# Performance work log

Measured on AMD Instinct MI355X. Metric: run time of the kernel, lower is better.

The kernel has to match this reference:

```python
import jax, jax.numpy as jnp
import numpy as np

BS, NA, NE_, NL = 128, 3, 3, 3
NALL = NA - 1                 # n_allies
ENT = NA + NE_ + NL           # 9 entities
EM1 = ENT - 1                 # 8
HID = 64                      # hidden_dim
HEAD = 4
HIN = 9                       # hyper input dim
HYP = 64                      # hyper hidden dim
NRBF, RUB = 3, 10.0
EPS = 1e-7


def _lin_init(k, fan_in, fan_out):
    k1, k2 = jax.random.split(k)
    lim = 1.0 / np.sqrt(fan_in)
    w = jax.random.uniform(k1, (fan_in, fan_out), minval=-lim, maxval=lim, dtype=jnp.float32)
    b = jax.random.uniform(k2, (fan_out,), minval=-lim, maxval=lim, dtype=jnp.float32)
    return w, b


def setup_inputs():
    key = jax.random.key(0)
    ks = jax.random.split(key, 12)
    d = {}
    obs_dim = 4 + 2 * (NL + NALL + NE_) + 2 * (NALL + NE_)  # 30
    d["inputs"] = jax.random.normal(ks[0], (BS * NA, obs_dim), dtype=jnp.float32)
    d["hidden_state"] = jnp.zeros((1, HID), dtype=jnp.float32)
    d["actions"] = jax.random.normal(ks[1], (BS * NA, 2), dtype=jnp.float32)
    out_dim = (HIN + 1) * HID * HEAD  # 2560
    d["hA1_w"], d["hA1_b"] = _lin_init(ks[2], HIN, HYP)
    d["hA2_w"], d["hA2_b"] = _lin_init(ks[3], HYP, out_dim)
    d["hE1_w"], d["hE1_b"] = _lin_init(ks[4], HIN, HYP)
    d["hE2_w"], d["hE2_b"] = _lin_init(ks[5], HYP, out_dim)
    d["hL1_w"], d["hL1_b"] = _lin_init(ks[6], HIN, HYP)
    d["hL2_w"], d["hL2_b"] = _lin_init(ks[7], HYP, out_dim)
    d["merger_w"] = jnp.ones((1, HEAD, HID), dtype=jnp.float32)
    d["fc1_w"], d["fc1_b"] = _lin_init(ks[8], HID + 3, HID)
    d["fc2_w"], d["fc2_b"] = _lin_init(ks[9], HID, 1)
    return d


def _pair_out(feat, w1, b1, w2, b2):
    # hypernetwork: Linear(9,64) -> LeakyReLU -> Linear(64, (9+1)*64*4)
    h = jax.nn.leaky_relu(feat @ w1 + b1, negative_slope=0.01)
    out = h @ w2 + b2                               # (bs,NA,EM1,EM1,2560)
    nw = HIN * HID * HEAD
    w = out[..., :nw].reshape(feat.shape[:-1] + (HIN, HID * HEAD))
    b = out[..., nw:]
    y = jnp.einsum('...k,...kd->...d', feat, w) + b  # tiny 1x9 @ 9x256 per pair
    return y.reshape(feat.shape[:-1] + (HEAD, HID))


def _forward(inputs, actions, hA1_w, hA1_b, hA2_w, hA2_b, hE1_w, hE1_b, hE2_w, hE2_b,
             hL1_w, hL1_b, hL2_w, hL2_b, merger_w, fc1_w, fc1_b, fc2_w, fc2_b):
    bs = inputs.shape[0] // NA
    ob = inputs
    own = ob[:, :4].reshape(bs, NA, 4)
    i = 4
    lm_pos = ob[:, i:i + NL * 2].reshape(bs, NA, NL, 2); i += NL * 2
    ally_pos = ob[:, i:i + NALL * 2].reshape(bs, NA, NALL, 2); i += NALL * 2
    enemy_pos = ob[:, i:i + NE_ * 2].reshape(bs, NA, NE_, 2); i += NE_ * 2
    entity_pos = jnp.concatenate([ally_pos, enemy_pos, lm_pos], axis=-2)  # (bs,NA,EM1,2)
    ally_vel = ob[:, i:i + NALL * 2].reshape(bs, NA, NALL, 2); i += NALL * 2
    enemy_vel = ob[:, i:i + NE_ * 2].reshape(bs, NA, NE_, 2)
    lm_vel = jnp.zeros_like(lm_pos) - own[:, :, None, :2]
    entity_vel = jnp.concatenate([ally_vel, enemy_vel, lm_vel], axis=-2)  # (bs,NA,EM1,2)
    # rel_vel[b,a,j,i] = vel[i] - vel[j]
    rel_vel = entity_vel[:, :, None, :, :] - entity_vel[:, :, :, None, :]
    vel_norm = jnp.sqrt((entity_vel ** 2).sum(-1))
    sin_a = entity_vel[..., 1] / (vel_norm + EPS)
    cos_a = entity_vel[..., 0] / (vel_norm + EPS)
    act = actions.reshape(bs, NA, 2)
    act_norm = jnp.sqrt((act ** 2).sum(-1))        # (bs,NA)
    sin_b = act[..., 1] / (act_norm + EPS)
    cos_b = act[..., 0] / (act_norm + EPS)
    dist = jnp.sqrt((entity_pos ** 2).sum(-1))     # (bs,NA,EM1)
    sin_t = entity_pos[..., 1] / (dist + EPS)
    cos_t = entity_pos[..., 0] / (dist + EPS)
    # pair angles: A,C vary over last axis (i), B over second-to-last (j)
    sA, cA = sin_t[:, :, None, :], cos_t[:, :, None, :]
    sB, cB = sin_t[:, :, :, None], cos_t[:, :, :, None]
    sC, cC = sin_a[:, :, None, :], cos_a[:, :, None, :]
    angle_info = jnp.stack([sA * cB - cA * sB, cA * cB + sA * sB,
                            sC * cB - cC * sB, cC * cB + sC * sB], axis=-1)
    angle_info = jnp.broadcast_to(angle_info, (bs, NA, EM1, EM1, 4))
    sD, cD = sin_b[:, :, None], cos_b[:, :, None]
    act_angle = jnp.stack([sD * cos_t - cD * sin_t, cD * cos_t + sD * sin_t], axis=-1)  # (bs,NA,EM1,2)
    # gaussian RBF (schnet-style smearing, num_rbf=3, rbound_upper=10)
    offset = jnp.linspace(0.0, RUB, NRBF)
    coeff = -0.5 / (offset[1] - offset[0]) ** 2
    rbf = jnp.exp(coeff * (dist[..., None] - offset) ** 2)  # (bs,NA,EM1,NRBF)
    feat_dist = jnp.broadcast_to(rbf[:, :, None, :, :], (bs, NA, EM1, EM1, NRBF))
    feat = jnp.concatenate([feat_dist, angle_info, rel_vel], axis=-1)  # (bs,NA,EM1,EM1,9)
    ally_out = _pair_out(feat, hA1_w, hA1_b, hA2_w, hA2_b)
    enemy_out = _pair_out(feat, hE1_w, hE1_b, hE2_w, hE2_b)
    lm_out = _pair_out(feat, hL1_w, hL1_b, hL2_w, hL2_b)
    # type-based selection over the source-entity axis (dim 3), then sum-aggregate
    m = jnp.concatenate([ally_out[:, :, :, :NALL],
                         enemy_out[:, :, :, NALL:NALL + NE_],
                         lm_out[:, :, :, NALL + NE_:]], axis=3)
    m_sum = m.sum(axis=3)                               # (bs,NA,EM1,HEAD,HID)
    mw = jax.nn.softmax(merger_w, axis=1)               # (1,HEAD,HID)
    m_jki = (mw * m_sum).sum(axis=-2)                   # (bs,NA,EM1,HID)
    an = jnp.broadcast_to(act_norm[:, :, None], (bs, NA, EM1))[..., None]
    final = jnp.concatenate([m_jki, an, act_angle], axis=-1)  # (bs,NA,EM1,HID+3)
    x = jax.nn.relu(final)
    x = jax.nn.relu(x @ fc1_w + fc1_b)
    q = (x @ fc2_w + fc2_b).mean(axis=-2).reshape(-1, 1)  # (bs*NA,1)
    return q, x


def reference(inputs, hidden_state, actions, hA1_w, hA1_b, hA2_w, hA2_b,
              hE1_w, hE1_b, hE2_w, hE2_b, hL1_w, hL1_b, hL2_w, hL2_b,
              merger_w, fc1_w, fc1_b, fc2_w, fc2_b):
    q, x = _forward(inputs, actions, hA1_w, hA1_b, hA2_w, hA2_b,
                    hE1_w, hE1_b, hE2_w, hE2_b, hL1_w, hL1_b, hL2_w, hL2_b,
                    merger_w, fc1_w, fc1_b, fc2_w, fc2_b)
    return q, x
```

## Files before the change

### kernel.cpp

```cpp
#include <hip/hip_runtime.h>
#include <math.h>

#define EPS 1e-7f
#define NETS 3
#define HROWP 384
#define HG    (HROWP/4)
#define GPW   (HG/4)
#define JSTRIDE (NETS*HROWP)
#define W2R_F4_TOT (2*NETS*HG*64)

__global__ __launch_bounds__(256) void prep_w2r(
    const float* __restrict__ W2A, const float* __restrict__ b2A,
    const float* __restrict__ W2E, const float* __restrict__ b2E,
    const float* __restrict__ W2L, const float* __restrict__ b2L,
    const float* __restrict__ merger, float* __restrict__ W2r)
{
    int idx = blockIdx.x * 256 + threadIdx.x;
    if (idx >= W2R_F4_TOT) return;
    int half = idx / (NETS*HG*64);
    int rem  = idx - half * (NETS*HG*64);
    int net  = rem / (HG*64);
    rem     -= net * (HG*64);
    int g4   = rem >> 6;
    int hid  = rem & 63;

    float m0 = merger[hid], m1 = merger[64+hid], m2 = merger[128+hid], m3 = merger[192+hid];
    float mx = fmaxf(fmaxf(m0, m1), fmaxf(m2, m3));
    float e0 = expf(m0-mx), e1 = expf(m1-mx), e2 = expf(m2-mx), e3 = expf(m3-mx);
    float inv = 1.0f / (e0+e1+e2+e3);
    float w0 = e0*inv, w1 = e1*inv, w2 = e2*inv, w3 = e3*inv;

    const float* W2 = (net==0) ? W2A : ((net==1) ? W2E : W2L);
    const float* b2 = (net==0) ? b2A : ((net==1) ? b2E : b2L);

    float4 v;
    float* vp = &v.x;
    #pragma unroll
    for (int r = 0; r < 4; ++r) {
        int row = g4*4 + r;
        float val = 0.0f;
        if (row < 325) {
            const float* src;
            int kk;
            if (row < 320) { kk = half*5 + (row >> 6); int h = row & 63; src = W2 + h*2560; }
            else           { kk = half*5 + (row - 320);                  src = b2; }
            int col = (kk < 9) ? kk*256 : 2304;
            val = w0*src[col+hid] + w1*src[col+64+hid] + w2*src[col+128+hid] + w3*src[col+192+hid];
        }
        vp[r] = val;
    }
    ((float4*)W2r)[idx] = v;
}

__global__ __launch_bounds__(256, 3) void half_kernel(
    const float* __restrict__ inputs, const float* __restrict__ actions,
    const float* __restrict__ W1A, const float* __restrict__ b1A,
    const float* __restrict__ W1E, const float* __restrict__ b1E,
    const float* __restrict__ W1L, const float* __restrict__ b1L,
    const float* __restrict__ W2r, float* __restrict__ Zpart)
{
    __shared__ float sOb[32];
    __shared__ float sSt[8], sCt[8], sSa[8], sCa[8], sVx[8], sVy[8];
    __shared__ float sRbf[8][3];
    __shared__ float sF[64][10];
    __shared__ __align__(16) float sU[8 * JSTRIDE];
    __shared__ float sZp[4][8][64];

    const int tid   = threadIdx.x;
    const int agent = blockIdx.x >> 1;
    const int half  = blockIdx.x & 1;

    if (tid < 30) sOb[tid] = inputs[agent*30 + tid];
    if (tid == 30) sOb[30] = actions[agent*2 + 0];
    if (tid == 31) sOb[31] = actions[agent*2 + 1];
    __syncthreads();

    if (tid < 8) {
        int e = tid;
        float px, py, vx, vy;
        if (e < 2)      {           px = sOb[10+2*e]; py = sOb[11+2*e]; vx = sOb[20+2*e]; vy = sOb[21+2*e]; }
        else if (e < 5) { int t=e-2; px = sOb[14+2*t]; py = sOb[15+2*t]; vx = sOb[24+2*t]; vy = sOb[25+2*t]; }
        else            { int t=e-5; px = sOb[4+2*t];  py = sOb[5+2*t];  vx = -sOb[0];     vy = -sOb[1]; }
        float d  = sqrtf(px*px + py*py);
        sSt[e] = py / (d + EPS);
        sCt[e] = px / (d + EPS);
        float vn = sqrtf(vx*vx + vy*vy);
        sSa[e] = vy / (vn + EPS);
        sCa[e] = vx / (vn + EPS);
        sVx[e] = vx; sVy[e] = vy;
        sRbf[e][0] = expf(-0.02f * d * d);
        float d5  = d - 5.0f;  sRbf[e][1] = expf(-0.02f * d5  * d5);
        float d10 = d - 10.0f; sRbf[e][2] = expf(-0.02f * d10 * d10);
    }
    __syncthreads();

    if (tid < 64) {
        int p = tid, j = p >> 3, k = p & 7;
        sF[p][0] = sRbf[k][0];
        sF[p][1] = sRbf[k][1];
        sF[p][2] = sRbf[k][2];
        sF[p][3] = sSt[k]*sCt[j] - sCt[k]*sSt[j];
        sF[p][4] = sCt[k]*sCt[j] + sSt[k]*sSt[j];
        sF[p][5] = sSa[k]*sCt[j] - sCa[k]*sSt[j];
        sF[p][6] = sCa[k]*sCt[j] + sSa[k]*sSt[j];
        sF[p][7] = sVx[k] - sVx[j];
        sF[p][8] = sVy[k] - sVy[j];
        sF[p][9] = 1.0f;
    }
    __syncthreads();

    for (int e = tid; e < 1536; e += 256) {
        int j = e / 192, rem = e - j*192;
        int net = rem >> 6, r = rem & 63;
        float v = 0.0f;
        if (r < 5) {
            int kk = half*5 + r;
            int ks = (net==0) ? 0 : ((net==1) ? 2 : 5);
            int kn = (net==0) ? 2 : 3;
            for (int q = 0; q < kn; ++q) v += sF[j*8 + ks + q][kk];
        }
        sU[(j*NETS + net)*HROWP + 320 + r] = v;
    }
    for (int e = tid; e < 1536; e += 256) {
        int j = e / 192, rem = e - j*192;
        int net = rem >> 6, h = rem & 63;
        int ks = (net==0) ? 0 : ((net==1) ? 2 : 5);
        int kn = (net==0) ? 2 : 3;
        const float* W1 = (net==0) ? W1A : ((net==1) ? W1E : W1L);
        const float* b1 = (net==0) ? b1A : ((net==1) ? b1E : b1L);
        float v[5];
        #pragma unroll
        for (int c = 0; c < 5; ++c) v[c] = 0.0f;
        for (int q = 0; q < kn; ++q) {
            int p = j*8 + ks + q;
            float acc = b1[h];
            #pragma unroll
            for (int kk = 0; kk < 9; ++kk) acc = fmaf(sF[p][kk], W1[kk*64 + h], acc);
            float H = (acc > 0.0f) ? acc : 0.01f*acc;
            #pragma unroll
            for (int c = 0; c < 5; ++c) v[c] = fmaf(H, sF[p][half*5 + c], v[c]);
        }
        float* dst = sU + (j*NETS + net)*HROWP + h;
        #pragma unroll
        for (int c = 0; c < 5; ++c) dst[c*64] = v[c];
    }
    __syncthreads();

    {
        const int lane = tid & 63, w = tid >> 6;
        const int q = lane >> 4, hh = lane & 15;
        const int base = w * GPW;
        float acc[8][4];
        #pragma unroll
        for (int j = 0; j < 8; ++j)
            #pragma unroll
            for (int k = 0; k < 4; ++k) acc[j][k] = 0.0f;

        const float4* Wbase = (const float4*)W2r + (size_t)half * (NETS*HG*64);

        float4 wk0, wk1, wk2, wk3, cu[8];
        {
            int g = base + q;
            const float4* wb = Wbase + g*64 + hh;
            wk0 = wb[0]; wk1 = wb[16]; wk2 = wb[32]; wk3 = wb[48];
            const float* Ub = sU + g*4;
            #pragma unroll
            for (int j = 0; j < 8; ++j) cu[j] = *(const float4*)(Ub + j*JSTRIDE);
        }
        for (int it = 0; it < 18; ++it) {
            float4 nk0, nk1, nk2, nk3, nu[8];
            if (it < 17) {
                int nit = it + 1;
                int nnet = nit / 6, nu_ = nit - nnet*6;
                int ng = base + nu_*4 + q;
                const float4* wb = Wbase + (nnet*HG + ng)*64 + hh;
                nk0 = wb[0]; nk1 = wb[16]; nk2 = wb[32]; nk3 = wb[48];
                const float* Ub = sU + nnet*HROWP + ng*4;
                #pragma unroll
                for (int j = 0; j < 8; ++j) nu[j] = *(const float4*)(Ub + j*JSTRIDE);
            }
            #pragma unroll
            for (int j = 0; j < 8; ++j) {
                float4 uu = cu[j];
                acc[j][0] = fmaf(uu.x,wk0.x, fmaf(uu.y,wk0.y, fmaf(uu.z,wk0.z, fmaf(uu.w,wk0.w, acc[j][0]))));
                acc[j][1] = fmaf(uu.x,wk1.x, fmaf(uu.y,wk1.y, fmaf(uu.z,wk1.z, fmaf(uu.w,wk1.w, acc[j][1]))));
                acc[j][2] = fmaf(uu.x,wk2.x, fmaf(uu.y,wk2.y, fmaf(uu.z,wk2.z, fmaf(uu.w,wk2.w, acc[j][2]))));
                acc[j][3] = fmaf(uu.x,wk3.x, fmaf(uu.y,wk3.y, fmaf(uu.z,wk3.z, fmaf(uu.w,wk3.w, acc[j][3]))));
            }
            wk0 = nk0; wk1 = nk1; wk2 = nk2; wk3 = nk3;
            #pragma unroll
            for (int j = 0; j < 8; ++j) cu[j] = nu[j];
        }
        #pragma unroll
        for (int j = 0; j < 8; ++j) {
            #pragma unroll
            for (int k = 0; k < 4; ++k) {
                float v = acc[j][k];
                v += __shfl_xor(v, 16);
                v += __shfl_xor(v, 32);
                if (q == 0) sZp[w][j][k*16 + hh] = v;
            }
        }
    }
    __syncthreads();
    {
        float* dst = Zpart + (size_t)agent*1024 + half*512;
        for (int o = tid; o < 512; o += 256) {
            int j = o >> 6, c = o & 63;
            dst[o] = sZp[0][j][c] + sZp[1][j][c] + sZp[2][j][c] + sZp[3][j][c];
        }
    }
}

__global__ __launch_bounds__(256) void epilogue_kernel(
    const float* __restrict__ inputs, const float* __restrict__ actions,
    const float* __restrict__ Zpart,
    const float* __restrict__ fc1w, const float* __restrict__ fc1b,
    const float* __restrict__ fc2w, const float* __restrict__ fc2b,
    float* __restrict__ out_q, float* __restrict__ out_x)
{
    __shared__ float sOb[32];
    __shared__ float sSt[8], sCt[8];
    __shared__ float sAct[3];
    __shared__ float sZ[8][64];
    __shared__ float sRed[4];

    const int tid   = threadIdx.x;
    const int agent = blockIdx.x;

    if (tid < 30) sOb[tid] = inputs[agent*30 + tid];
    if (tid == 30) sOb[30] = actions[agent*2 + 0];
    if (tid == 31) sOb[31] = actions[agent*2 + 1];
    __syncthreads();

    if (tid < 8) {
        int e = tid;
        float px, py;
        if (e < 2)      {           px = sOb[10+2*e]; py = sOb[11+2*e]; }
        else if (e < 5) { int t=e-2; px = sOb[14+2*t]; py = sOb[15+2*t]; }
        else            { int t=e-5; px = sOb[4+2*t];  py = sOb[5+2*t]; }
        float d = sqrtf(px*px + py*py);
        sSt[e] = py / (d + EPS);
        sCt[e] = px / (d + EPS);
    }
    if (tid == 8) {
        float ax = sOb[30], ay = sOb[31];
        float an = sqrtf(ax*ax + ay*ay);
        sAct[0] = an;
        sAct[1] = ay / (an + EPS);
        sAct[2] = ax / (an + EPS);
    }
    const float* Zp = Zpart + (size_t)agent*1024;
    for (int o = tid; o < 512; o += 256) {
        float z = Zp[o] + Zp[512 + o];
        ((float*)sZ)[o] = (z > 0.0f) ? z : 0.0f;
    }
    __syncthreads();

    float an  = sAct[0], sb = sAct[1], cb = sAct[2];
    float anr = (an > 0.0f) ? an : 0.0f;
    float myq = 0.0f;
    #pragma unroll
    for (int i = 0; i < 2; ++i) {
        int o = i*256 + tid;
        int j = o >> 6, c = o & 63;
        float acc = fc1b[c];
        #pragma unroll 8
        for (int d = 0; d < 64; ++d)
            acc = fmaf(sZ[j][d], fc1w[d*64 + c], acc);
        float aa0 = sb*sCt[j] - cb*sSt[j];
        float aa1 = cb*sCt[j] + sb*sSt[j];
        aa0 = (aa0 > 0.0f) ? aa0 : 0.0f;
        aa1 = (aa1 > 0.0f) ? aa1 : 0.0f;
        acc = fmaf(anr, fc1w[64*64 + c], acc);
        acc = fmaf(aa0, fc1w[65*64 + c], acc);
        acc = fmaf(aa1, fc1w[66*64 + c], acc);
        float x1 = (acc > 0.0f) ? acc : 0.0f;
        out_x[(agent*8 + j)*64 + c] = x1;
        myq = fmaf(x1, fc2w[c], myq);
    }
    for (int off = 32; off; off >>= 1) myq += __shfl_down(myq, off);
    int lane = tid & 63, w = tid >> 6;
    if (lane == 0) sRed[w] = myq;
    __syncthreads();
    if (tid == 0) out_q[agent] = (sRed[0] + sRed[1] + sRed[2] + sRed[3]) * 0.125f + fc2b[0];
}

extern "C" void kernel_launch(void* const* d_in, const int* in_sizes, int n_in,
                              void* d_out, int out_size, void* d_ws, size_t ws_size,
                              hipStream_t stream) {
    const float* inputs  = (const float*)d_in[0];
    const float* actions = (const float*)d_in[2];
    const float* hA1_w = (const float*)d_in[3];  const float* hA1_b = (const float*)d_in[4];
    const float* hA2_w = (const float*)d_in[5];  const float* hA2_b = (const float*)d_in[6];
    const float* hE1_w = (const float*)d_in[7];  const float* hE1_b = (const float*)d_in[8];
    const float* hE2_w = (const float*)d_in[9];  const float* hE2_b = (const float*)d_in[10];
    const float* hL1_w = (const float*)d_in[11]; const float* hL1_b = (const float*)d_in[12];
    const float* hL2_w = (const float*)d_in[13]; const float* hL2_b = (const float*)d_in[14];
    const float* merger = (const float*)d_in[15];
    const float* fc1w = (const float*)d_in[16];  const float* fc1b = (const float*)d_in[17];
    const float* fc2w = (const float*)d_in[18];  const float* fc2b = (const float*)d_in[19];

    float* W2r   = (float*)d_ws;
    float* Zpart = (float*)((char*)d_ws + 589824);
    float* q     = (float*)d_out;
    float* x     = q + 384;

    prep_w2r<<<(W2R_F4_TOT + 255)/256, 256, 0, stream>>>(
        hA2_w, hA2_b, hE2_w, hE2_b, hL2_w, hL2_b, merger, W2r);
    half_kernel<<<768, 256, 0, stream>>>(
        inputs, actions, hA1_w, hA1_b, hE1_w, hE1_b, hL1_w, hL1_b, W2r, Zpart);
    epilogue_kernel<<<384, 256, 0, stream>>>(
        inputs, actions, Zpart, fc1w, fc1b, fc2w, fc2b, q, x);
}
```

Measured before the change: 122.1 us.

## Fuse epilogue into half kernel via last-block atomic counter

Removes the separate epilogue launch. The second of the two half-blocks per agent, detected with an atomic counter, now sums the partial Z and runs fc1/fc2. It also stages the W1/b1 weights in shared memory and merges the two sU-fill loops into one pass. The main loop now reads the U operands straight from shared memory each iteration instead of prefetching them into registers, which lowers register pressure. The cost is fences and atomics, the counter reset folded into prep_w2r, extra shared memory for sW1, and more LDS traffic in the inner loop.

```diff
diff --git a/kernel.cpp b/kernel.cpp
--- a/kernel.cpp
+++ b/kernel.cpp
@@ -8,14 +8,18 @@
 #define GPW   (HG/4)
 #define JSTRIDE (NETS*HROWP)
 #define W2R_F4_TOT (2*NETS*HG*64)
+#define ZPART_OFF 589824
+#define ZCNT_OFF  2162688
 
 __global__ __launch_bounds__(256) void prep_w2r(
     const float* __restrict__ W2A, const float* __restrict__ b2A,
     const float* __restrict__ W2E, const float* __restrict__ b2E,
     const float* __restrict__ W2L, const float* __restrict__ b2L,
-    const float* __restrict__ merger, float* __restrict__ W2r)
+    const float* __restrict__ merger, float* __restrict__ W2r,
+    int* __restrict__ Zcnt)
 {
     int idx = blockIdx.x * 256 + threadIdx.x;
+    if (idx < 384) Zcnt[idx] = 0;
     if (idx >= W2R_F4_TOT) return;
     int half = idx / (NETS*HG*64);
     int rem  = idx - half * (NETS*HG*64);
@@ -57,14 +61,21 @@
     const float* __restrict__ W1A, const float* __restrict__ b1A,
     const float* __restrict__ W1E, const float* __restrict__ b1E,
     const float* __restrict__ W1L, const float* __restrict__ b1L,
-    const float* __restrict__ W2r, float* __restrict__ Zpart)
+    const float* __restrict__ W2r, float* __restrict__ Zpart,
+    int* __restrict__ Zcnt,
+    const float* __restrict__ fc1w, const float* __restrict__ fc1b,
+    const float* __restrict__ fc2w, const float* __restrict__ fc2b,
+    float* __restrict__ out_q, float* __restrict__ out_x)
 {
     __shared__ float sOb[32];
     __shared__ float sSt[8], sCt[8], sSa[8], sCa[8], sVx[8], sVy[8];
     __shared__ float sRbf[8][3];
+    __shared__ float sAct[3];
     __shared__ float sF[64][10];
+    __shared__ float sW1[NETS*640];
     __shared__ __align__(16) float sU[8 * JSTRIDE];
-    __shared__ float sZp[4][8][64];
+    __shared__ float sRed[4];
+    __shared__ int   sIsLast;
 
     const int tid   = threadIdx.x;
     const int agent = blockIdx.x >> 1;
@@ -73,6 +84,13 @@
     if (tid < 30) sOb[tid] = inputs[agent*30 + tid];
     if (tid == 30) sOb[30] = actions[agent*2 + 0];
     if (tid == 31) sOb[31] = actions[agent*2 + 1];
+    for (int i = tid; i < 480; i += 256) {
+        int net = i / 160, r = i - net*160;
+        const float* W1 = (net==0) ? W1A : ((net==1) ? W1E : W1L);
+        const float* b1 = (net==0) ? b1A : ((net==1) ? b1E : b1L);
+        const float4 v = (r < 144) ? ((const float4*)W1)[r] : ((const float4*)b1)[r-144];
+        ((float4*)(sW1 + net*640))[r] = v;
+    }
     __syncthreads();
 
     if (tid < 8) {
@@ -92,6 +110,13 @@
         float d5  = d - 5.0f;  sRbf[e][1] = expf(-0.02f * d5  * d5);
         float d10 = d - 10.0f; sRbf[e][2] = expf(-0.02f * d10 * d10);
     }
+    if (tid == 8) {
+        float ax = sOb[30], ay = sOb[31];
+        float an = sqrtf(ax*ax + ay*ay);
+        sAct[0] = an;
+        sAct[1] = ay / (an + EPS);
+        sAct[2] = ax / (an + EPS);
+    }
     __syncthreads();
 
     if (tid < 64) {
@@ -109,43 +134,45 @@
     }
     __syncthreads();
 
-    for (int e = tid; e < 1536; e += 256) {
-        int j = e / 192, rem = e - j*192;
-        int net = rem >> 6, r = rem & 63;
-        float v = 0.0f;
-        if (r < 5) {
-            int kk = half*5 + r;
+    for (int e = tid; e < 3072; e += 256) {
+        if (e < 1536) {
+            int j = e / 192, rem = e - j*192;
+            int net = rem >> 6, h = rem & 63;
             int ks = (net==0) ? 0 : ((net==1) ? 2 : 5);
             int kn = (net==0) ? 2 : 3;
-            for (int q = 0; q < kn; ++q) v += sF[j*8 + ks + q][kk];
-        }
-        sU[(j*NETS + net)*HROWP + 320 + r] = v;
-    }
-    for (int e = tid; e < 1536; e += 256) {
-        int j = e / 192, rem = e - j*192;
-        int net = rem >> 6, h = rem & 63;
-        int ks = (net==0) ? 0 : ((net==1) ? 2 : 5);
-        int kn = (net==0) ? 2 : 3;
-        const float* W1 = (net==0) ? W1A : ((net==1) ? W1E : W1L);
-        const float* b1 = (net==0) ? b1A : ((net==1) ? b1E : b1L);
-        float v[5];
-        #pragma unroll
-        for (int c = 0; c < 5; ++c) v[c] = 0.0f;
-        for (int q = 0; q < kn; ++q) {
-            int p = j*8 + ks + q;
-            float acc = b1[h];
-            #pragma unroll
-            for (int kk = 0; kk < 9; ++kk) acc = fmaf(sF[p][kk], W1[kk*64 + h], acc);
-            float H = (acc > 0.0f) ? acc : 0.01f*acc;
-            #pragma unroll
-            for (int c = 0; c < 5; ++c) v[c] = fmaf(H, sF[p][half*5 + c], v[c]);
-        }
-        float* dst = sU + (j*NETS + net)*HROWP + h;
-        #pragma unroll
-        for (int c = 0; c < 5; ++c) dst[c*64] = v[c];
-    }
-    __syncthreads();
-
+            const float* w1 = sW1 + net*640;
+            float v[5];
+            #pragma unroll
+            for (int c = 0; c < 5; ++c) v[c] = 0.0f;
+            for (int q = 0; q < kn; ++q) {
+                int p = j*8 + ks + q;
+                float acc = w1[576 + h];
+                #pragma unroll
+                for (int kk = 0; kk < 9; ++kk) acc = fmaf(sF[p][kk], w1[kk*64 + h], acc);
+                float H = (acc > 0.0f) ? acc : 0.01f*acc;
+                #pragma unroll
+                for (int c = 0; c < 5; ++c) v[c] = fmaf(H, sF[p][half*5 + c], v[c]);
+            }
+            float* dst = sU + (j*NETS + net)*HROWP + h;
+            #pragma unroll
+            for (int c = 0; c < 5; ++c) dst[c*64] = v[c];
+        } else {
+            int t = e - 1536;
+            int j = t / 192, rem = t - j*192;
+            int net = rem >> 6, r = rem & 63;
+            float v = 0.0f;
+            if (r < 5) {
+                int kk = half*5 + r;
+                int ks = (net==0) ? 0 : ((net==1) ? 2 : 5);
+                int kn = (net==0) ? 2 : 3;
+                for (int q = 0; q < kn; ++q) v += sF[j*8 + ks + q][kk];
+            }
+            sU[(j*NETS + net)*HROWP + 320 + r] = v;
+        }
+    }
+    __syncthreads();
+
+    float vr[8][4];
     {
         const int lane = tid & 63, w = tid >> 6;
         const int q = lane >> 4, hh = lane & 15;
@@ -157,133 +184,111 @@
             for (int k = 0; k < 4; ++k) acc[j][k] = 0.0f;
 
         const float4* Wbase = (const float4*)W2r + (size_t)half * (NETS*HG*64);
-
-        float4 wk0, wk1, wk2, wk3, cu[8];
-        {
-            int g = base + q;
+        float4 wk0, wk1, wk2, wk3;
+        {   int g = base + q;
             const float4* wb = Wbase + g*64 + hh;
-            wk0 = wb[0]; wk1 = wb[16]; wk2 = wb[32]; wk3 = wb[48];
-            const float* Ub = sU + g*4;
-            #pragma unroll
-            for (int j = 0; j < 8; ++j) cu[j] = *(const float4*)(Ub + j*JSTRIDE);
-        }
+            wk0 = wb[0]; wk1 = wb[16]; wk2 = wb[32]; wk3 = wb[48]; }
+
         for (int it = 0; it < 18; ++it) {
-            float4 nk0, nk1, nk2, nk3, nu[8];
+            int net = it / 6, u = it - net*6;
+            int g = base + u*4 + q;
+            float4 nk0, nk1, nk2, nk3;
             if (it < 17) {
                 int nit = it + 1;
                 int nnet = nit / 6, nu_ = nit - nnet*6;
                 int ng = base + nu_*4 + q;
                 const float4* wb = Wbase + (nnet*HG + ng)*64 + hh;
                 nk0 = wb[0]; nk1 = wb[16]; nk2 = wb[32]; nk3 = wb[48];
-                const float* Ub = sU + nnet*HROWP + ng*4;
-                #pragma unroll
-                for (int j = 0; j < 8; ++j) nu[j] = *(const float4*)(Ub + j*JSTRIDE);
-            }
+            }
+            const float* Ub = sU + net*HROWP + g*4;
             #pragma unroll
             for (int j = 0; j < 8; ++j) {
-                float4 uu = cu[j];
+                float4 uu = *(const float4*)(Ub + j*JSTRIDE);
                 acc[j][0] = fmaf(uu.x,wk0.x, fmaf(uu.y,wk0.y, fmaf(uu.z,wk0.z, fmaf(uu.w,wk0.w, acc[j][0]))));
                 acc[j][1] = fmaf(uu.x,wk1.x, fmaf(uu.y,wk1.y, fmaf(uu.z,wk1.z, fmaf(uu.w,wk1.w, acc[j][1]))));
                 acc[j][2] = fmaf(uu.x,wk2.x, fmaf(uu.y,wk2.y, fmaf(uu.z,wk2.z, fmaf(uu.w,wk2.w, acc[j][2]))));
                 acc[j][3] = fmaf(uu.x,wk3.x, fmaf(uu.y,wk3.y, fmaf(uu.z,wk3.z, fmaf(uu.w,wk3.w, acc[j][3]))));
             }
             wk0 = nk0; wk1 = nk1; wk2 = nk2; wk3 = nk3;
-            #pragma unroll
-            for (int j = 0; j < 8; ++j) cu[j] = nu[j];
         }
         #pragma unroll
-        for (int j = 0; j < 8; ++j) {
+        for (int j = 0; j < 8; ++j)
             #pragma unroll
             for (int k = 0; k < 4; ++k) {
                 float v = acc[j][k];
                 v += __shfl_xor(v, 16);
                 v += __shfl_xor(v, 32);
-                if (q == 0) sZp[w][j][k*16 + hh] = v;
-            }
-        }
-    }
-    __syncthreads();
-    {
+                vr[j][k] = v;
+            }
+    }
+    __syncthreads();
+    {
+        float* sZp = sU;
+        const int lane = tid & 63, w = tid >> 6;
+        const int q = lane >> 4, hh = lane & 15;
+        if (q == 0) {
+            #pragma unroll
+            for (int j = 0; j < 8; ++j)
+                #pragma unroll
+                for (int k = 0; k < 4; ++k)
+                    sZp[(w*8 + j)*64 + k*16 + hh] = vr[j][k];
+        }
+    }
+    __syncthreads();
+    {
+        const float* sZp = sU;
         float* dst = Zpart + (size_t)agent*1024 + half*512;
+        for (int o = tid; o < 512; o += 256)
+            dst[o] = sZp[o] + sZp[512+o] + sZp[1024+o] + sZp[1536+o];
+    }
+    __threadfence();
+    __syncthreads();
+    if (tid == 0) {
+        int old = atomicAdd(&Zcnt[agent], 1);
+        sIsLast = (old == 1);
+    }
+    __syncthreads();
+    if (!sIsLast) return;
+    __threadfence();
+
+    float* sZ = sU + 2048;
+    {
+        const float* Zp = Zpart + (size_t)agent*1024;
         for (int o = tid; o < 512; o += 256) {
+            float z = Zp[o] + Zp[512 + o];
+            sZ[o] = (z > 0.0f) ? z : 0.0f;
+        }
+    }
+    __syncthreads();
+    {
+        float an  = sAct[0], sb = sAct[1], cb = sAct[2];
+        float anr = (an > 0.0f) ? an : 0.0f;
+        float myq = 0.0f;
+        #pragma unroll
+        for (int i = 0; i < 2; ++i) {
+            int o = i*256 + tid;
             int j = o >> 6, c = o & 63;
-            dst[o] = sZp[0][j][c] + sZp[1][j][c] + sZp[2][j][c] + sZp[3][j][c];
-        }
-    }
-}
-
-__global__ __launch_bounds__(256) void epilogue_kernel(
-    const float* __restrict__ inputs, const float* __restrict__ actions,
-    const float* __restrict__ Zpart,
-    const float* __restrict__ fc1w, const float* __restrict__ fc1b,
-    const float* __restrict__ fc2w, const float* __restrict__ fc2b,
-    float* __restrict__ out_q, float* __restrict__ out_x)
-{
-    __shared__ float sOb[32];
-    __shared__ float sSt[8], sCt[8];
-    __shared__ float sAct[3];
-    __shared__ float sZ[8][64];
-    __shared__ float sRed[4];
-
-    const int tid   = threadIdx.x;
-    const int agent = blockIdx.x;
-
-    if (tid < 30) sOb[tid] = inputs[agent*30 + tid];
-    if (tid == 30) sOb[30] = actions[agent*2 + 0];
-    if (tid == 31) sOb[31] = actions[agent*2 + 1];
-    __syncthreads();
-
-    if (tid < 8) {
-        int e = tid;
-        float px, py;
-        if (e < 2)      {           px = sOb[10+2*e]; py = sOb[11+2*e]; }
-        else if (e < 5) { int t=e-2; px = sOb[14+2*t]; py = sOb[15+2*t]; }
-        else            { int t=e-5; px = sOb[4+2*t];  py = sOb[5+2*t]; }
-        float d = sqrtf(px*px + py*py);
-        sSt[e] = py / (d + EPS);
-        sCt[e] = px / (d + EPS);
-    }
-    if (tid == 8) {
-        float ax = sOb[30], ay = sOb[31];
-        float an = sqrtf(ax*ax + ay*ay);
-        sAct[0] = an;
-        sAct[1] = ay / (an + EPS);
-        sAct[2] = ax / (an + EPS);
-    }
-    const float* Zp = Zpart + (size_t)agent*1024;
-    for (int o = tid; o < 512; o += 256) {
-        float z = Zp[o] + Zp[512 + o];
-        ((float*)sZ)[o] = (z > 0.0f) ? z : 0.0f;
-    }
-    __syncthreads();
-
-    float an  = sAct[0], sb = sAct[1], cb = sAct[2];
-    float anr = (an > 0.0f) ? an : 0.0f;
-    float myq = 0.0f;
-    #pragma unroll
-    for (int i = 0; i < 2; ++i) {
-        int o = i*256 + tid;
-        int j = o >> 6, c = o & 63;
-        float acc = fc1b[c];
-        #pragma unroll 8
-        for (int d = 0; d < 64; ++d)
-            acc = fmaf(sZ[j][d], fc1w[d*64 + c], acc);
-        float aa0 = sb*sCt[j] - cb*sSt[j];
-        float aa1 = cb*sCt[j] + sb*sSt[j];
-        aa0 = (aa0 > 0.0f) ? aa0 : 0.0f;
-        aa1 = (aa1 > 0.0f) ? aa1 : 0.0f;
-        acc = fmaf(anr, fc1w[64*64 + c], acc);
-        acc = fmaf(aa0, fc1w[65*64 + c], acc);
-        acc = fmaf(aa1, fc1w[66*64 + c], acc);
-        float x1 = (acc > 0.0f) ? acc : 0.0f;
-        out_x[(agent*8 + j)*64 + c] = x1;
-        myq = fmaf(x1, fc2w[c], myq);
-    }
-    for (int off = 32; off; off >>= 1) myq += __shfl_down(myq, off);
-    int lane = tid & 63, w = tid >> 6;
-    if (lane == 0) sRed[w] = myq;
-    __syncthreads();
-    if (tid == 0) out_q[agent] = (sRed[0] + sRed[1] + sRed[2] + sRed[3]) * 0.125f + fc2b[0];
+            float acc = fc1b[c];
+            #pragma unroll 8
+            for (int d = 0; d < 64; ++d)
+                acc = fmaf(sZ[j*64 + d], fc1w[d*64 + c], acc);
+            float aa0 = sb*sCt[j] - cb*sSt[j];
+            float aa1 = cb*sCt[j] + sb*sSt[j];
+            aa0 = (aa0 > 0.0f) ? aa0 : 0.0f;
+            aa1 = (aa1 > 0.0f) ? aa1 : 0.0f;
+            acc = fmaf(anr, fc1w[64*64 + c], acc);
+            acc = fmaf(aa0, fc1w[65*64 + c], acc);
+            acc = fmaf(aa1, fc1w[66*64 + c], acc);
+            float x1 = (acc > 0.0f) ? acc : 0.0f;
+            out_x[(agent*8 + j)*64 + c] = x1;
+            myq = fmaf(x1, fc2w[c], myq);
+        }
+        for (int off = 32; off; off >>= 1) myq += __shfl_down(myq, off);
+        int lane = tid & 63, w = tid >> 6;
+        if (lane == 0) sRed[w] = myq;
+        __syncthreads();
+        if (tid == 0) out_q[agent] = (sRed[0] + sRed[1] + sRed[2] + sRed[3]) * 0.125f + fc2b[0];
+    }
 }
 
 extern "C" void kernel_launch(void* const* d_in, const int* in_sizes, int n_in,
@@ -302,14 +307,14 @@
     const float* fc2w = (const float*)d_in[18];  const float* fc2b = (const float*)d_in[19];
 
     float* W2r   = (float*)d_ws;
-    float* Zpart = (float*)((char*)d_ws + 589824);
+    float* Zpart = (float*)((char*)d_ws + ZPART_OFF);
+    int*   Zcnt  = (int*)  ((char*)d_ws + ZCNT_OFF);
     float* q     = (float*)d_out;
     float* x     = q + 384;
 
     prep_w2r<<<(W2R_F4_TOT + 255)/256, 256, 0, stream>>>(
-        hA2_w, hA2_b, hE2_w, hE2_b, hL2_w, hL2_b, merger, W2r);
+        hA2_w, hA2_b, hE2_w, hE2_b, hL2_w, hL2_b, merger, W2r, Zcnt);
     half_kernel<<<768, 256, 0, stream>>>(
-        inputs, actions, hA1_w, hA1_b, hE1_w, hE1_b, hL1_w, hL1_b, W2r, Zpart);
-    epilogue_kernel<<<384, 256, 0, stream>>>(
-        inputs, actions, Zpart, fc1w, fc1b, fc2w, fc2b, q, x);
+        inputs, actions, hA1_w, hA1_b, hE1_w, hE1_b, hL1_w, hL1_b,
+        W2r, Zpart, Zcnt, fc1w, fc1b, fc2w, fc2b, q, x);
 }
```

Result: slower. 198.0 us (+62.2%).

## Register-cache W1 weights, restructure hidden stage, reuse sU for partial sums

Applied to the files above, without the earlier changes.

Each thread now preloads its lane's hyper-network first-layer weights and biases into registers. The hidden-layer stage is remapped so each wave handles two target entities with vectorized float4 reads of padded features, and the bias rows are folded in alongside. The software prefetch of U rows from LDS into registers is dropped in favour of direct LDS reads, and the sZp buffer is aliased onto sU to cut shared-memory footprint. The aim is fewer global loads of W1, lower register and LDS pressure, and higher occupancy. The cost is an extra barrier and LDS read latency that is no longer hidden by prefetch.

```diff
diff --git a/kernel.cpp b/kernel.cpp
--- a/kernel.cpp
+++ b/kernel.cpp
@@ -8,6 +8,7 @@
 #define GPW   (HG/4)
 #define JSTRIDE (NETS*HROWP)
 #define W2R_F4_TOT (2*NETS*HG*64)
+#define ZPART_OFF 589824
 
 __global__ __launch_bounds__(256) void prep_w2r(
     const float* __restrict__ W2A, const float* __restrict__ b2A,
@@ -62,13 +63,26 @@
     __shared__ float sOb[32];
     __shared__ float sSt[8], sCt[8], sSa[8], sCa[8], sVx[8], sVy[8];
     __shared__ float sRbf[8][3];
-    __shared__ float sF[64][10];
+    __shared__ __align__(16) float sF2[64][12];
     __shared__ __align__(16) float sU[8 * JSTRIDE];
-    __shared__ float sZp[4][8][64];
 
     const int tid   = threadIdx.x;
     const int agent = blockIdx.x >> 1;
     const int half  = blockIdx.x & 1;
+    const int lane  = tid & 63;
+    const int w     = tid >> 6;
+
+    float w1r[3][9], b1r[3];
+    {
+        const float* Ws[3] = {W1A, W1E, W1L};
+        const float* bs[3] = {b1A, b1E, b1L};
+        #pragma unroll
+        for (int net = 0; net < 3; ++net) {
+            #pragma unroll
+            for (int kk = 0; kk < 9; ++kk) w1r[net][kk] = Ws[net][kk*64 + lane];
+            b1r[net] = bs[net][lane];
+        }
+    }
 
     if (tid < 30) sOb[tid] = inputs[agent*30 + tid];
     if (tid == 30) sOb[30] = actions[agent*2 + 0];
@@ -96,58 +110,80 @@
 
     if (tid < 64) {
         int p = tid, j = p >> 3, k = p & 7;
-        sF[p][0] = sRbf[k][0];
-        sF[p][1] = sRbf[k][1];
-        sF[p][2] = sRbf[k][2];
-        sF[p][3] = sSt[k]*sCt[j] - sCt[k]*sSt[j];
-        sF[p][4] = sCt[k]*sCt[j] + sSt[k]*sSt[j];
-        sF[p][5] = sSa[k]*sCt[j] - sCa[k]*sSt[j];
-        sF[p][6] = sCa[k]*sCt[j] + sSa[k]*sSt[j];
-        sF[p][7] = sVx[k] - sVx[j];
-        sF[p][8] = sVy[k] - sVy[j];
-        sF[p][9] = 1.0f;
-    }
-    __syncthreads();
-
-    for (int e = tid; e < 1536; e += 256) {
-        int j = e / 192, rem = e - j*192;
-        int net = rem >> 6, r = rem & 63;
-        float v = 0.0f;
-        if (r < 5) {
-            int kk = half*5 + r;
-            int ks = (net==0) ? 0 : ((net==1) ? 2 : 5);
-            int kn = (net==0) ? 2 : 3;
-            for (int q = 0; q < kn; ++q) v += sF[j*8 + ks + q][kk];
-        }
-        sU[(j*NETS + net)*HROWP + 320 + r] = v;
-    }
-    for (int e = tid; e < 1536; e += 256) {
-        int j = e / 192, rem = e - j*192;
-        int net = rem >> 6, h = rem & 63;
-        int ks = (net==0) ? 0 : ((net==1) ? 2 : 5);
-        int kn = (net==0) ? 2 : 3;
-        const float* W1 = (net==0) ? W1A : ((net==1) ? W1E : W1L);
-        const float* b1 = (net==0) ? b1A : ((net==1) ? b1E : b1L);
-        float v[5];
+        sF2[p][0] = sRbf[k][0];
+        sF2[p][1] = sRbf[k][1];
+        sF2[p][2] = sRbf[k][2];
+        sF2[p][3] = sSt[k]*sCt[j] - sCt[k]*sSt[j];
+        sF2[p][4] = sCt[k]*sCt[j] + sSt[k]*sSt[j];
+        sF2[p][5] = sSa[k]*sCt[j] - sCa[k]*sSt[j];
+        sF2[p][6] = sCa[k]*sCt[j] + sSa[k]*sSt[j];
+        sF2[p][7] = sVx[k] - sVx[j];
+        sF2[p][8] = sVy[k] - sVy[j];
+        sF2[p][9] = 1.0f;
+        sF2[p][10] = 0.0f;
+        sF2[p][11] = 0.0f;
+    }
+    __syncthreads();
+
+    {
+        const int h = lane;
         #pragma unroll
-        for (int c = 0; c < 5; ++c) v[c] = 0.0f;
-        for (int q = 0; q < kn; ++q) {
-            int p = j*8 + ks + q;
-            float acc = b1[h];
-            #pragma unroll
-            for (int kk = 0; kk < 9; ++kk) acc = fmaf(sF[p][kk], W1[kk*64 + h], acc);
-            float H = (acc > 0.0f) ? acc : 0.01f*acc;
-            #pragma unroll
-            for (int c = 0; c < 5; ++c) v[c] = fmaf(H, sF[p][half*5 + c], v[c]);
-        }
-        float* dst = sU + (j*NETS + net)*HROWP + h;
-        #pragma unroll
-        for (int c = 0; c < 5; ++c) dst[c*64] = v[c];
-    }
-    __syncthreads();
-
-    {
-        const int lane = tid & 63, w = tid >> 6;
+        for (int t = 0; t < 2; ++t) {
+            int j = 2*w + t;
+            #pragma unroll
+            for (int net = 0; net < NETS; ++net) {
+                int ks = (net==0) ? 0 : ((net==1) ? 2 : 5);
+                int kn = (net==0) ? 2 : 3;
+                float v0=0.f,v1=0.f,v2=0.f,v3=0.f,v4=0.f;
+                float gs0=0.f,gs1=0.f,gs2=0.f,gs3=0.f,gs4=0.f;
+                for (int q = 0; q < kn; ++q) {
+                    int p = j*8 + ks + q;
+                    float4 fa = *(const float4*)&sF2[p][0];
+                    float4 fb = *(const float4*)&sF2[p][4];
+                    float4 fc = *(const float4*)&sF2[p][8];
+                    float acc = b1r[net];
+                    acc = fmaf(fa.x, w1r[net][0], acc);
+                    acc = fmaf(fa.y, w1r[net][1], acc);
+                    acc = fmaf(fa.z, w1r[net][2], acc);
+                    acc = fmaf(fa.w, w1r[net][3], acc);
+                    acc = fmaf(fb.x, w1r[net][4], acc);
+                    acc = fmaf(fb.y, w1r[net][5], acc);
+                    acc = fmaf(fb.z, w1r[net][6], acc);
+                    acc = fmaf(fb.w, w1r[net][7], acc);
+                    acc = fmaf(fc.x, w1r[net][8], acc);
+                    float H = (acc > 0.0f) ? acc : 0.01f*acc;
+                    float g0 = half ? fb.y : fa.x;
+                    float g1 = half ? fb.z : fa.y;
+                    float g2 = half ? fb.w : fa.z;
+                    float g3 = half ? fc.x : fa.w;
+                    float g4 = half ? fc.y : fb.x;
+                    v0 = fmaf(H, g0, v0);  gs0 += g0;
+                    v1 = fmaf(H, g1, v1);  gs1 += g1;
+                    v2 = fmaf(H, g2, v2);  gs2 += g2;
+                    v3 = fmaf(H, g3, v3);  gs3 += g3;
+                    v4 = fmaf(H, g4, v4);  gs4 += g4;
+                }
+                float* dst = sU + (j*NETS + net)*HROWP + h;
+                dst[0]   = v0;
+                dst[64]  = v1;
+                dst[128] = v2;
+                dst[192] = v3;
+                dst[256] = v4;
+                float bv = 0.0f;
+                bv = (h==0) ? gs0 : bv;
+                bv = (h==1) ? gs1 : bv;
+                bv = (h==2) ? gs2 : bv;
+                bv = (h==3) ? gs3 : bv;
+                bv = (h==4) ? gs4 : bv;
+                dst[320 - h + h] = bv;
+                sU[(j*NETS + net)*HROWP + 320 + h] = bv;
+            }
+        }
+    }
+    __syncthreads();
+
+    float vr[8][4];
+    {
         const int q = lane >> 4, hh = lane & 15;
         const int base = w * GPW;
         float acc[8][4];
@@ -157,58 +193,61 @@
             for (int k = 0; k < 4; ++k) acc[j][k] = 0.0f;
 
         const float4* Wbase = (const float4*)W2r + (size_t)half * (NETS*HG*64);
-
-        float4 wk0, wk1, wk2, wk3, cu[8];
-        {
-            int g = base + q;
+        float4 wk0, wk1, wk2, wk3;
+        {   int g = base + q;
             const float4* wb = Wbase + g*64 + hh;
-            wk0 = wb[0]; wk1 = wb[16]; wk2 = wb[32]; wk3 = wb[48];
-            const float* Ub = sU + g*4;
-            #pragma unroll
-            for (int j = 0; j < 8; ++j) cu[j] = *(const float4*)(Ub + j*JSTRIDE);
-        }
+            wk0 = wb[0]; wk1 = wb[16]; wk2 = wb[32]; wk3 = wb[48]; }
+
         for (int it = 0; it < 18; ++it) {
-            float4 nk0, nk1, nk2, nk3, nu[8];
+            int net = it / 6, u = it - net*6;
+            int g = base + u*4 + q;
+            float4 nk0, nk1, nk2, nk3;
             if (it < 17) {
                 int nit = it + 1;
                 int nnet = nit / 6, nu_ = nit - nnet*6;
                 int ng = base + nu_*4 + q;
                 const float4* wb = Wbase + (nnet*HG + ng)*64 + hh;
                 nk0 = wb[0]; nk1 = wb[16]; nk2 = wb[32]; nk3 = wb[48];
-                const float* Ub = sU + nnet*HROWP + ng*4;
-                #pragma unroll
-                for (int j = 0; j < 8; ++j) nu[j] = *(const float4*)(Ub + j*JSTRIDE);
             }
+            const float* Ub = sU + net*HROWP + g*4;
             #pragma unroll
             for (int j = 0; j < 8; ++j) {
-                float4 uu = cu[j];
+                float4 uu = *(const float4*)(Ub + j*JSTRIDE);
                 acc[j][0] = fmaf(uu.x,wk0.x, fmaf(uu.y,wk0.y, fmaf(uu.z,wk0.z, fmaf(uu.w,wk0.w, acc[j][0]))));
                 acc[j][1] = fmaf(uu.x,wk1.x, fmaf(uu.y,wk1.y, fmaf(uu.z,wk1.z, fmaf(uu.w,wk1.w, acc[j][1]))));
                 acc[j][2] = fmaf(uu.x,wk2.x, fmaf(uu.y,wk2.y, fmaf(uu.z,wk2.z, fmaf(uu.w,wk2.w, acc[j][2]))));
                 acc[j][3] = fmaf(uu.x,wk3.x, fmaf(uu.y,wk3.y, fmaf(uu.z,wk3.z, fmaf(uu.w,wk3.w, acc[j][3]))));
             }
             wk0 = nk0; wk1 = nk1; wk2 = nk2; wk3 = nk3;
-            #pragma unroll
-            for (int j = 0; j < 8; ++j) cu[j] = nu[j];
         }
         #pragma unroll
-        for (int j = 0; j < 8; ++j) {
+        for (int j = 0; j < 8; ++j)
             #pragma unroll
             for (int k = 0; k < 4; ++k) {
                 float v = acc[j][k];
                 v += __shfl_xor(v, 16);
                 v += __shfl_xor(v, 32);
-                if (q == 0) sZp[w][j][k*16 + hh] = v;
+                vr[j][k] = v;
             }
-        }
-    }
-    __syncthreads();
-    {
+    }
+    __syncthreads();
+    {
+        float* sZp = sU;
+        const int q = lane >> 4, hh = lane & 15;
+        if (q == 0) {
+            #pragma unroll
+            for (int j = 0; j < 8; ++j)
+                #pragma unroll
+                for (int k = 0; k < 4; ++k)
+                    sZp[(w*8 + j)*64 + k*16 + hh] = vr[j][k];
+        }
+    }
+    __syncthreads();
+    {
+        const float* sZp = sU;
         float* dst = Zpart + (size_t)agent*1024 + half*512;
-        for (int o = tid; o < 512; o += 256) {
-            int j = o >> 6, c = o & 63;
-            dst[o] = sZp[0][j][c] + sZp[1][j][c] + sZp[2][j][c] + sZp[3][j][c];
-        }
+        for (int o = tid; o < 512; o += 256)
+            dst[o] = sZp[o] + sZp[512+o] + sZp[1024+o] + sZp[1536+o];
     }
 }
 
@@ -302,7 +341,7 @@
     const float* fc2w = (const float*)d_in[18];  const float* fc2b = (const float*)d_in[19];
 
     float* W2r   = (float*)d_ws;
-    float* Zpart = (float*)((char*)d_ws + 589824);
+    float* Zpart = (float*)((char*)d_ws + ZPART_OFF);
     float* q     = (float*)d_out;
     float* x     = q + 384;
 
```

After: 120.0 us. No clear change (-1.7%).
